# Kernel optimization log

Measured on AMD Instinct MI355X. Metric: run time of the kernel, lower is better.

Reference implementation:

```python
import jax, jax.numpy as jnp
import numpy as np

DIM = 1024
H = 16
HD = DIM // H  # 64
B, N = 2, 2048
EPS = 1e-6


def setup_inputs() -> dict:
    key = jax.random.key(0)
    ks = jax.random.split(key, 12)
    s = 0.02
    return {
        "x": jax.random.normal(ks[0], (B, N, DIM), jnp.float32),
        "rotary_cos": jax.random.uniform(ks[1], (B, N, HD), jnp.float32),
        "rotary_sin": jax.random.uniform(ks[2], (B, N, HD), jnp.float32),
        "Wq": jax.random.normal(ks[3], (DIM, DIM), jnp.float32) * s,
        "bq": jnp.zeros((DIM,), jnp.float32),
        "Wk": jax.random.normal(ks[4], (DIM, DIM), jnp.float32) * s,
        "bk": jnp.zeros((DIM,), jnp.float32),
        "Wv": jax.random.normal(ks[5], (DIM, DIM), jnp.float32) * s,
        "bv": jnp.zeros((DIM,), jnp.float32),
        "q_norm_w": jnp.ones((HD,), jnp.float32),
        "q_norm_b": jnp.zeros((HD,), jnp.float32),
        "k_norm_w": jnp.ones((HD,), jnp.float32),
        "k_norm_b": jnp.zeros((HD,), jnp.float32),
        "Wo": jax.random.normal(ks[6], (DIM, DIM), jnp.float32) * s,
        "bo": jnp.zeros((DIM,), jnp.float32),
    }


def _layernorm(x, w, b):
    mu = jnp.mean(x, axis=-1, keepdims=True)
    var = jnp.mean(jnp.square(x - mu), axis=-1, keepdims=True)
    return (x - mu) * jax.lax.rsqrt(var + EPS) * w + b


def _rotate_half(x):
    x1, x2 = jnp.split(x, 2, axis=-1)
    return jnp.concatenate((-x2, x1), axis=-1)


def _apply_rope(x, cos, sin):
    # x: [B,H,N,D]; cos/sin: [B,N,D] -> [B,1,N,D]
    cos = cos[:, None]
    sin = sin[:, None]
    return x * cos + _rotate_half(x) * sin


def reference(x, rotary_cos, rotary_sin, Wq, bq, Wk, bk, Wv, bv,
              q_norm_w, q_norm_b, k_norm_w, k_norm_b, Wo, bo):
    b, n, c = x.shape
    q = x @ Wq + bq
    k = x @ Wk + bk
    v = x @ Wv + bv
    # Faithful packed-qkv permutation: cat -> view(.., H, 3*hd) -> split(hd)
    qkv = jnp.concatenate((q, k, v), axis=-1).reshape(b, n, H, 3 * HD)
    q, k, v = jnp.split(qkv, 3, axis=-1)  # each [B,N,H,HD]
    q = q.transpose(0, 2, 1, 3)  # [B,H,N,HD]
    k = k.transpose(0, 2, 1, 3)
    v = v.transpose(0, 2, 1, 3)
    q = _layernorm(q, q_norm_w, q_norm_b)
    k = _layernorm(k, k_norm_w, k_norm_b)
    q = _apply_rope(q, rotary_cos, rotary_sin)
    k = _apply_rope(k, rotary_cos, rotary_sin)
    scale = HD ** -0.5
    scores = jnp.einsum("bhqd,bhkd->bhqk", q, k) * scale
    probs = jax.nn.softmax(scores, axis=-1)
    out = jnp.einsum("bhqk,bhkd->bhqd", probs, v)
    out = out.transpose(0, 2, 1, 3).reshape(b, n, c)
    return out @ Wo + bo
```

## Files before the change

### kernel.cpp

```cpp
#include <hip/hip_runtime.h>

typedef __attribute__((ext_vector_type(8))) __bf16 bf16x8;
typedef __attribute__((ext_vector_type(4))) float  f32x4;

#define DEV __device__ __forceinline__

DEV void async_copy16(const void* g, void* l) {
  __builtin_amdgcn_global_load_lds((const __attribute__((address_space(1))) void*)g,
                                   (__attribute__((address_space(3))) void*)l, 16, 0, 0);
}

DEV float ldf(const void* p, size_t i, int isbf) {
  if (isbf) {
    unsigned int w = ((unsigned int)((const unsigned short*)p)[i]) << 16;
    float f; __builtin_memcpy(&f, &w, 4); return f;
  }
  return ((const float*)p)[i];
}

DEV int detect_isbf(const unsigned short* __restrict__ x) {
  int bad = 0;
#pragma unroll
  for (int i = 0; i < 64; i++) {
    int e = (x[i] >> 7) & 0xFF;
    bad |= (e >= 0x90) ? 1 : 0;
  }
  return !bad;
}

__global__ __launch_bounds__(256) void prep(const void* __restrict__ Wq,
                                            const void* __restrict__ Wk,
                                            const void* __restrict__ Wv,
                                            const void* __restrict__ Wo,
                                            const void* __restrict__ x,
                                            const void* __restrict__ bq,
                                            const void* __restrict__ bk,
                                            const void* __restrict__ bv,
                                            const void* __restrict__ bo,
                                            __bf16* __restrict__ Wt,
                                            __bf16* __restrict__ Wot,
                                            __bf16* __restrict__ x_bf,
                                            float* __restrict__ bias) {
  __shared__ float tile[32][33];
  const int isbf = detect_isbf((const unsigned short*)x);
  const int tid = threadIdx.x;
  const int z = blockIdx.z;

  if (z < 4) {
    const void* in = (z == 0) ? Wq : (z == 1) ? Wk : (z == 2) ? Wv : Wo;
    __bf16* out = (z < 3) ? (Wt + (size_t)z * 1024 * 1024) : Wot;
    const int tx = tid & 31, ty = tid >> 5;
    const int r0 = blockIdx.y * 32, c0 = blockIdx.x * 32;
#pragma unroll
    for (int i = 0; i < 4; i++) {
      int r = ty + i * 8;
      tile[r][tx] = ldf(in, (size_t)(r0 + r) * 1024 + c0 + tx, isbf);
    }
    __syncthreads();
#pragma unroll
    for (int i = 0; i < 4; i++) {
      int r = ty + i * 8;
      out[(size_t)(c0 + r) * 1024 + r0 + tx] = (__bf16)tile[tx][r];
    }
  } else {
    const int id = blockIdx.y * 32 + blockIdx.x;
    if (!isbf) {
#pragma unroll
      for (int j = 0; j < 4; j++) {
        int idx = id * 1024 + j * 256 + tid;
        float4 f = ((const float4*)x)[idx];
        union { __bf16 h[4]; uint2 u; } pk;
        pk.h[0] = (__bf16)f.x; pk.h[1] = (__bf16)f.y;
        pk.h[2] = (__bf16)f.z; pk.h[3] = (__bf16)f.w;
        ((uint2*)x_bf)[idx] = pk.u;
      }
    }
    if (id < 16) {
      int i = id * 256 + tid;
      if (i < 1024)      bias[i] = ldf(bq, i, isbf);
      else if (i < 2048) bias[i] = ldf(bk, i - 1024, isbf);
      else if (i < 3072) bias[i] = ldf(bv, i - 2048, isbf);
      else               bias[i] = ldf(bo, i - 3072, isbf);
    }
  }
}

template <int DYN, int NT, int ALT>
__global__ __launch_bounds__(256, 3) void gemm_bt(const __bf16* __restrict__ A,
                                                  const __bf16* __restrict__ Aalt,
                                                  const __bf16* __restrict__ Bt,
                                                  const float* __restrict__ bias,
                                                  void* __restrict__ Cout,
                                                  const unsigned short* __restrict__ xdet,
                                                  int M, int N, int K) {
  constexpr int WN = NT / 2;
  constexpr int JB = WN / 16;
  constexpr int NR = NT / 32;
  __shared__ __align__(16) __bf16 As[128 * 64];
  __shared__ __align__(16) __bf16 Bs[NT * 64];
  const int tid = threadIdx.x;
  const int wid = tid >> 6, lane = tid & 63;
  const int m_blk = blockIdx.x * 128, n_blk = blockIdx.y * NT;
  const int wm = (wid & 1) * 64, wn = (wid >> 1) * WN;
  const int l8 = lane >> 3, l7 = lane & 7;
  const int cc = l7 ^ (l8 & 7);
  const int q4 = lane >> 4, l15 = lane & 15;

  int isbf = 1;
  if (DYN || ALT) isbf = detect_isbf(xdet);
  const __bf16* Ap = (ALT && isbf) ? Aalt : A;

  f32x4 acc[4][JB] = {};

  for (int kb = 0; kb < K; kb += 64) {
    __syncthreads();
#pragma unroll
    for (int i = 0; i < 4; i++) {
      int row = i * 32 + wid * 8 + l8;
      async_copy16(Ap + (size_t)(m_blk + row) * K + kb + cc * 8,
                   As + (i * 32 + wid * 8) * 64);
    }
#pragma unroll
    for (int i = 0; i < NR; i++) {
      int row = i * 32 + wid * 8 + l8;
      async_copy16(Bt + (size_t)(n_blk + row) * K + kb + cc * 8,
                   Bs + (i * 32 + wid * 8) * 64);
    }
    __syncthreads();
#pragma unroll
    for (int k0 = 0; k0 < 64; k0 += 32) {
      bf16x8 a[4], b[JB];
#pragma unroll
      for (int i = 0; i < 4; i++) {
        int ra = wm + i * 16 + l15;
        int ba = ra * 8 + (((k0 >> 3) + q4) ^ (ra & 7));
        a[i] = *(const bf16x8*)&As[ba * 8];
      }
#pragma unroll
      for (int j = 0; j < JB; j++) {
        int rb = wn + j * 16 + l15;
        int bb = rb * 8 + (((k0 >> 3) + q4) ^ (rb & 7));
        b[j] = *(const bf16x8*)&Bs[bb * 8];
      }
#pragma unroll
      for (int i = 0; i < 4; i++)
#pragma unroll
        for (int j = 0; j < JB; j++)
          acc[i][j] = __builtin_amdgcn_mfma_f32_16x16x32_bf16(a[i], b[j], acc[i][j], 0, 0, 0);
    }
  }

  float bcol[JB];
#pragma unroll
  for (int j = 0; j < JB; j++) bcol[j] = bias[n_blk + wn + j * 16 + l15];
#pragma unroll
  for (int i = 0; i < 4; i++)
#pragma unroll
    for (int j = 0; j < JB; j++) {
      int col = n_blk + wn + j * 16 + l15;
#pragma unroll
      for (int r = 0; r < 4; r++) {
        int row = m_blk + wm + i * 16 + q4 * 4 + r;
        float v = acc[i][j][r] + bcol[j];
        size_t idx = (size_t)row * N + col;
        if (DYN && !isbf) ((float*)Cout)[idx] = v;
        else              ((__bf16*)Cout)[idx] = (__bf16)v;
      }
    }
}

__global__ __launch_bounds__(256) void ln_rope_v(const __bf16* __restrict__ qkv,
                                                 const void* __restrict__ rcos,
                                                 const void* __restrict__ rsin,
                                                 const void* __restrict__ qw,
                                                 const void* __restrict__ qb,
                                                 const void* __restrict__ kw,
                                                 const void* __restrict__ kb_,
                                                 const unsigned short* __restrict__ xdet,
                                                 __bf16* __restrict__ Qp,
                                                 __bf16* __restrict__ Kp,
                                                 __bf16* __restrict__ Vt) {
  __shared__ __bf16 vt[64][68];
  const int isbf = detect_isbf(xdet);
  const int tid = threadIdx.x, w = tid >> 6, lane = tid & 63;
  const int bh = blockIdx.y, h = bh & 15, b = bh >> 4;
  const int n0 = blockIdx.x * 64;

  float gq = ldf(qw, lane, isbf), bq_ = ldf(qb, lane, isbf);
  float gk = ldf(kw, lane, isbf), bk_ = ldf(kb_, lane, isbf);

#pragma unroll 2
  for (int t = 0; t < 16; t++) {
    const int n = n0 + w * 16 + t;
    const size_t tok = (size_t)b * 2048 + n;
    const __bf16* base = qkv + tok * 3072 + h * 192;
    float qv = (float)base[lane], kv = (float)base[64 + lane], vv = (float)base[128 + lane];

    float sq = qv, sk = kv;
#pragma unroll
    for (int m = 1; m < 64; m <<= 1) { sq += __shfl_xor(sq, m, 64); sk += __shfl_xor(sk, m, 64); }
    float muq = sq * (1.0f / 64.0f), muk = sk * (1.0f / 64.0f);
    float tq = qv - muq, tk = kv - muk;
    float vq = tq * tq, vk = tk * tk;
#pragma unroll
    for (int m = 1; m < 64; m <<= 1) { vq += __shfl_xor(vq, m, 64); vk += __shfl_xor(vk, m, 64); }
    float rsq = rsqrtf(vq * (1.0f / 64.0f) + 1e-6f);
    float rsk = rsqrtf(vk * (1.0f / 64.0f) + 1e-6f);
    float qn = tq * rsq * gq + bq_;
    float kn = tk * rsk * gk + bk_;

    float c = ldf(rcos, tok * 64 + lane, isbf), s = ldf(rsin, tok * 64 + lane, isbf);
    float qpart = __shfl_xor(qn, 32, 64), kpart = __shfl_xor(kn, 32, 64);
    float qrh = (lane < 32) ? -qpart : qpart;
    float krh = (lane < 32) ? -kpart : kpart;

    const size_t oidx = ((size_t)bh * 2048 + n) * 64 + lane;
    Qp[oidx] = (__bf16)((qn * c + qrh * s) * 0.1803368801111204f);
    Kp[oidx] = (__bf16)(kn * c + krh * s);
    vt[lane][w * 16 + t] = (__bf16)vv;
  }
  __syncthreads();
  const int row = tid >> 2, qt = tid & 3;
  size_t gbase = (size_t)bh * 64 * 2048 + (size_t)row * 2048 + n0 + qt * 16;
#pragma unroll
  for (int u = 0; u < 4; u++)
    *(uint2*)&Vt[gbase + u * 4] = *(const uint2*)&vt[row][qt * 16 + u * 4];
}

__global__ __launch_bounds__(256, 4) void attn(const __bf16* __restrict__ Qp,
                                               const __bf16* __restrict__ Kp,
                                               const __bf16* __restrict__ Vt,
                                               float* __restrict__ O0,
                                               float* __restrict__ O1,
                                               float* __restrict__ lpart) {
  __shared__ __align__(16) __bf16 sK[2][2048];
  __shared__ __align__(16) __bf16 sV[2][2048];
  __shared__ __align__(16) __bf16 sP[4][1024];

  const int tid = threadIdx.x, wid = tid >> 6, lane = tid & 63;
  const int q4 = lane >> 4, l15 = lane & 15;
  const int lin = blockIdx.x;
  const int xcd = lin & 7;
  const int rest = lin >> 3;
  const int qblk = rest & 15;
  const int g = (rest >> 4) * 8 + xcd;
  const int bh = g & 31, split = g >> 5;
  const int q0w = qblk * 128 + wid * 32;
  const int kt0 = split * 1024;
  const __bf16* Qb = Qp + (size_t)bh * 2048 * 64;
  const __bf16* Kb = Kp + (size_t)bh * 2048 * 64;
  const __bf16* Vb = Vt + (size_t)bh * 64 * 2048;
  float* Op = split ? O1 : O0;
  __bf16* sPw = &sP[wid][0];
  const int pbase = (q4 >> 1) * 128 + l15 * 8 + (q4 & 1) * 4;

  bf16x8 qf[2][2];
#pragma unroll
  for (int qs = 0; qs < 2; qs++)
#pragma unroll
    for (int c = 0; c < 2; c++)
      qf[qs][c] = *(const bf16x8*)&Qb[(size_t)(q0w + qs * 16 + l15) * 64 + c * 32 + q4 * 8];

  bf16x8 ones8;
#pragma unroll
  for (int i = 0; i < 8; i++) ones8[i] = (__bf16)1.0f;

  f32x4 o[2][4] = {};
  f32x4 l_acc[2] = {};

#define STAGE(kt, bf)                                                                    \
  do {                                                                                   \
    async_copy16(Kb + (size_t)((kt) + (wid >> 1) * 16 + l15) * 64 + (wid & 1) * 32 + q4 * 8, \
                 &sK[bf][wid * 512]);                                                    \
    async_copy16(Vb + (size_t)(wid * 16 + l15) * 2048 + (kt) + q4 * 8,                   \
                 &sV[bf][wid * 512]);                                                    \
  } while (0)

  STAGE(kt0, 0);

  for (int it = 0; it < 32; ++it) {
    const int buf = it & 1;
    __syncthreads();
    if (it < 31) STAGE(kt0 + (it + 1) * 32, buf ^ 1);

    bf16x8 ak[2][2];
#pragma unroll
    for (int ks = 0; ks < 2; ks++)
#pragma unroll
      for (int c = 0; c < 2; c++)
        ak[ks][c] = *(const bf16x8*)&sK[buf][((ks * 2 + c) * 64 + lane) * 8];
    f32x4 sc[2][2];
#pragma unroll
    for (int qs = 0; qs < 2; qs++)
#pragma unroll
      for (int ks = 0; ks < 2; ks++) {
        f32x4 z = {0.f, 0.f, 0.f, 0.f};
        z = __builtin_amdgcn_mfma_f32_16x16x32_bf16(ak[ks][0], qf[qs][0], z, 0, 0, 0);
        z = __builtin_amdgcn_mfma_f32_16x16x32_bf16(ak[ks][1], qf[qs][1], z, 0, 0, 0);
        sc[qs][ks] = z;
      }

#pragma unroll
    for (int qs = 0; qs < 2; qs++)
#pragma unroll
      for (int ks = 0; ks < 2; ks++) {
        uint2 pk;
        {
          float p0 = __builtin_amdgcn_exp2f(sc[qs][ks][0]);
          float p1 = __builtin_amdgcn_exp2f(sc[qs][ks][1]);
          pk.x = __builtin_amdgcn_perm(__builtin_bit_cast(unsigned int, p1),
                                       __builtin_bit_cast(unsigned int, p0), 0x07060302u);
          float p2 = __builtin_amdgcn_exp2f(sc[qs][ks][2]);
          float p3 = __builtin_amdgcn_exp2f(sc[qs][ks][3]);
          pk.y = __builtin_amdgcn_perm(__builtin_bit_cast(unsigned int, p3),
                                       __builtin_bit_cast(unsigned int, p2), 0x07060302u);
        }
        *(uint2*)&sPw[qs * 512 + ks * 256 + pbase] = pk;
      }
    asm volatile("s_waitcnt lgkmcnt(0)" ::: "memory");

    bf16x8 pb[2];
#pragma unroll
    for (int qs = 0; qs < 2; qs++)
      pb[qs] = *(const bf16x8*)&sPw[(qs * 64 + lane) * 8];
#pragma unroll
    for (int qs = 0; qs < 2; qs++)
      l_acc[qs] = __builtin_amdgcn_mfma_f32_16x16x32_bf16(ones8, pb[qs], l_acc[qs], 0, 0, 0);
#pragma unroll
    for (int ds = 0; ds < 4; ds++) {
      bf16x8 av = *(const bf16x8*)&sV[buf][(ds * 64 + lane) * 8];
#pragma unroll
      for (int qs = 0; qs < 2; qs++)
        o[qs][ds] = __builtin_amdgcn_mfma_f32_16x16x32_bf16(av, pb[qs], o[qs][ds], 0, 0, 0);
    }
  }
#undef STAGE

#pragma unroll
  for (int qs = 0; qs < 2; qs++) {
    const int q = q0w + qs * 16 + l15;
    if (q4 == 0) lpart[(size_t)(split * 32 + bh) * 2048 + q] = l_acc[qs][0];
    size_t base = ((size_t)bh * 2048 + q) * 64;
#pragma unroll
    for (int ds = 0; ds < 4; ds++)
      *(f32x4*)&Op[base + ds * 16 + q4 * 4] = o[qs][ds];
  }
}

__global__ __launch_bounds__(256) void combine(const float* __restrict__ O0,
                                               const float* __restrict__ O1,
                                               const float* __restrict__ lpart,
                                               __bf16* __restrict__ Obuf) {
  const int idx = blockIdx.x * 256 + threadIdx.x;
  const int d4 = idx & 15, q = (idx >> 4) & 2047, bh = idx >> 15;
  const int b = bh >> 4, h = bh & 15;
  const size_t po = ((size_t)bh * 2048 + q) * 64 + d4 * 4;
  f32x4 a = *(const f32x4*)&O0[po];
  f32x4 c = *(const f32x4*)&O1[po];
  float l = lpart[(size_t)bh * 2048 + q] + lpart[(size_t)(32 + bh) * 2048 + q];
  float rl = 1.0f / l;
  union { __bf16 h4[4]; uint2 u; } pk;
#pragma unroll
  for (int r = 0; r < 4; r++) pk.h4[r] = (__bf16)((a[r] + c[r]) * rl);
  *(uint2*)&Obuf[((size_t)(b * 2048 + q)) * 1024 + h * 64 + d4 * 4] = pk.u;
}

extern "C" void kernel_launch(void* const* d_in, const int* in_sizes, int n_in,
                              void* d_out, int out_size, void* d_ws, size_t ws_size,
                              hipStream_t stream) {
  const void* x   = d_in[0];
  const void* rc  = d_in[1];
  const void* rs  = d_in[2];
  const void* Wq  = d_in[3];
  const void* bq  = d_in[4];
  const void* Wk  = d_in[5];
  const void* bk  = d_in[6];
  const void* Wv  = d_in[7];
  const void* bv  = d_in[8];
  const void* qnw = d_in[9];
  const void* qnb = d_in[10];
  const void* knw = d_in[11];
  const void* knb = d_in[12];
  const void* Wo  = d_in[13];
  const void* bo  = d_in[14];
  const unsigned short* xdet = (const unsigned short*)x;

  char* ws = (char*)d_ws;
  __bf16* qkv   = (__bf16*)ws;
  float*  O0    = (float*)ws;
  float*  O1    = (float*)(ws + 16777216);
  __bf16* x_bf  = (__bf16*)(ws + 25165824);
  __bf16* Qp    = (__bf16*)(ws + 33554432);
  __bf16* Obuf  = (__bf16*)(ws + 33554432);
  __bf16* Kp    = (__bf16*)(ws + 41943040);
  __bf16* Vt    = (__bf16*)(ws + 50331648);
  __bf16* Wt    = (__bf16*)(ws + 58720256);
  __bf16* Wot   = (__bf16*)(ws + 65011712);
  float*  bias  = (float*)(ws + 67108864);
  float*  lprt  = (float*)(ws + 67125248);

  prep<<<dim3(32, 32, 5), 256, 0, stream>>>(Wq, Wk, Wv, Wo, x, bq, bk, bv, bo,
                                            Wt, Wot, x_bf, bias);
  gemm_bt<0, 128, 1><<<dim3(32, 24), 256, 0, stream>>>(x_bf, (const __bf16*)x, Wt, bias,
                                                       qkv, xdet, 4096, 3072, 1024);
  ln_rope_v<<<dim3(32, 32), 256, 0, stream>>>(qkv, rc, rs, qnw, qnb, knw, knb, xdet,
                                              Qp, Kp, Vt);
  attn<<<1024, 256, 0, stream>>>(Qp, Kp, Vt, O0, O1, lprt);
  combine<<<4096, 256, 0, stream>>>(O0, O1, lprt, Obuf);
  gemm_bt<1, 64, 0><<<dim3(32, 16), 256, 0, stream>>>(Obuf, nullptr, Wot, bias + 3072,
                                                      d_out, xdet, 4096, 1024, 1024);
}
```

Before: 235.4 us.

## Double attention query tile per wave and remap GEMM blocks by XCD

The attention kernel now gives each wave 64 query rows instead of 32, which halves the grid and reuses each staged K/V tile across twice as many queries. It also fuses the score MFMA with the exp/pack step per sub-tile. Both GEMMs switch to a 1D grid whose block index is remapped so each XCD works on a contiguous range of N columns, which should improve L2 reuse of weight tiles. The costs are more accumulator registers and a larger P buffer in attention, so occupancy drops (launch bound 2 instead of 4), and there are fewer blocks to hide latency.

```diff
diff --git a/kernel.cpp b/kernel.cpp
--- a/kernel.cpp
+++ b/kernel.cpp
@@ -85,7 +85,7 @@
   }
 }
 
-template <int DYN, int NT, int ALT>
+template <int DYN, int NT, int ALT, int NPX>
 __global__ __launch_bounds__(256, 3) void gemm_bt(const __bf16* __restrict__ A,
                                                   const __bf16* __restrict__ Aalt,
                                                   const __bf16* __restrict__ Bt,
@@ -100,7 +100,9 @@
   __shared__ __align__(16) __bf16 Bs[NT * 64];
   const int tid = threadIdx.x;
   const int wid = tid >> 6, lane = tid & 63;
-  const int m_blk = blockIdx.x * 128, n_blk = blockIdx.y * NT;
+  const int xcd = blockIdx.x & 7, t = blockIdx.x >> 3;
+  const int m_blk = (t & 31) * 128;
+  const int n_blk = (xcd * NPX + (t >> 5)) * NT;
   const int wm = (wid & 1) * 64, wn = (wid >> 1) * WN;
   const int l8 = lane >> 3, l7 = lane & 7;
   const int cc = l7 ^ (l8 & 7);
@@ -227,7 +229,7 @@
     *(uint2*)&Vt[gbase + u * 4] = *(const uint2*)&vt[row][qt * 16 + u * 4];
 }
 
-__global__ __launch_bounds__(256, 4) void attn(const __bf16* __restrict__ Qp,
+__global__ __launch_bounds__(256, 2) void attn(const __bf16* __restrict__ Qp,
                                                const __bf16* __restrict__ Kp,
                                                const __bf16* __restrict__ Vt,
                                                float* __restrict__ O0,
@@ -235,17 +237,15 @@
                                                float* __restrict__ lpart) {
   __shared__ __align__(16) __bf16 sK[2][2048];
   __shared__ __align__(16) __bf16 sV[2][2048];
-  __shared__ __align__(16) __bf16 sP[4][1024];
+  __shared__ __align__(16) __bf16 sP[4][2048];
 
   const int tid = threadIdx.x, wid = tid >> 6, lane = tid & 63;
   const int q4 = lane >> 4, l15 = lane & 15;
-  const int lin = blockIdx.x;
-  const int xcd = lin & 7;
-  const int rest = lin >> 3;
-  const int qblk = rest & 15;
-  const int g = (rest >> 4) * 8 + xcd;
+  const int xcd = blockIdx.x & 7, t = blockIdx.x >> 3;
+  const int qblk = t & 7;
+  const int g = xcd * 8 + (t >> 3);
   const int bh = g & 31, split = g >> 5;
-  const int q0w = qblk * 128 + wid * 32;
+  const int q0w = qblk * 256 + wid * 64;
   const int kt0 = split * 1024;
   const __bf16* Qb = Qp + (size_t)bh * 2048 * 64;
   const __bf16* Kb = Kp + (size_t)bh * 2048 * 64;
@@ -254,9 +254,9 @@
   __bf16* sPw = &sP[wid][0];
   const int pbase = (q4 >> 1) * 128 + l15 * 8 + (q4 & 1) * 4;
 
-  bf16x8 qf[2][2];
-#pragma unroll
-  for (int qs = 0; qs < 2; qs++)
+  bf16x8 qf[4][2];
+#pragma unroll
+  for (int qs = 0; qs < 4; qs++)
 #pragma unroll
     for (int c = 0; c < 2; c++)
       qf[qs][c] = *(const bf16x8*)&Qb[(size_t)(q0w + qs * 16 + l15) * 64 + c * 32 + q4 * 8];
@@ -265,8 +265,8 @@
 #pragma unroll
   for (int i = 0; i < 8; i++) ones8[i] = (__bf16)1.0f;
 
-  f32x4 o[2][4] = {};
-  f32x4 l_acc[2] = {};
+  f32x4 o[4][4] = {};
+  f32x4 l_acc[4] = {};
 
 #define STAGE(kt, bf)                                                                    \
   do {                                                                                   \
@@ -289,55 +289,49 @@
 #pragma unroll
       for (int c = 0; c < 2; c++)
         ak[ks][c] = *(const bf16x8*)&sK[buf][((ks * 2 + c) * 64 + lane) * 8];
-    f32x4 sc[2][2];
-#pragma unroll
-    for (int qs = 0; qs < 2; qs++)
+
+#pragma unroll
+    for (int qs = 0; qs < 4; qs++) {
 #pragma unroll
       for (int ks = 0; ks < 2; ks++) {
         f32x4 z = {0.f, 0.f, 0.f, 0.f};
         z = __builtin_amdgcn_mfma_f32_16x16x32_bf16(ak[ks][0], qf[qs][0], z, 0, 0, 0);
         z = __builtin_amdgcn_mfma_f32_16x16x32_bf16(ak[ks][1], qf[qs][1], z, 0, 0, 0);
-        sc[qs][ks] = z;
-      }
-
-#pragma unroll
-    for (int qs = 0; qs < 2; qs++)
-#pragma unroll
-      for (int ks = 0; ks < 2; ks++) {
         uint2 pk;
         {
-          float p0 = __builtin_amdgcn_exp2f(sc[qs][ks][0]);
-          float p1 = __builtin_amdgcn_exp2f(sc[qs][ks][1]);
+          float p0 = __builtin_amdgcn_exp2f(z[0]);
+          float p1 = __builtin_amdgcn_exp2f(z[1]);
           pk.x = __builtin_amdgcn_perm(__builtin_bit_cast(unsigned int, p1),
                                        __builtin_bit_cast(unsigned int, p0), 0x07060302u);
-          float p2 = __builtin_amdgcn_exp2f(sc[qs][ks][2]);
-          float p3 = __builtin_amdgcn_exp2f(sc[qs][ks][3]);
+          float p2 = __builtin_amdgcn_exp2f(z[2]);
+          float p3 = __builtin_amdgcn_exp2f(z[3]);
           pk.y = __builtin_amdgcn_perm(__builtin_bit_cast(unsigned int, p3),
                                        __builtin_bit_cast(unsigned int, p2), 0x07060302u);
         }
         *(uint2*)&sPw[qs * 512 + ks * 256 + pbase] = pk;
       }
+    }
     asm volatile("s_waitcnt lgkmcnt(0)" ::: "memory");
 
-    bf16x8 pb[2];
-#pragma unroll
-    for (int qs = 0; qs < 2; qs++)
+    bf16x8 pb[4];
+#pragma unroll
+    for (int qs = 0; qs < 4; qs++)
       pb[qs] = *(const bf16x8*)&sPw[(qs * 64 + lane) * 8];
 #pragma unroll
-    for (int qs = 0; qs < 2; qs++)
+    for (int qs = 0; qs < 4; qs++)
       l_acc[qs] = __builtin_amdgcn_mfma_f32_16x16x32_bf16(ones8, pb[qs], l_acc[qs], 0, 0, 0);
 #pragma unroll
     for (int ds = 0; ds < 4; ds++) {
       bf16x8 av = *(const bf16x8*)&sV[buf][(ds * 64 + lane) * 8];
 #pragma unroll
-      for (int qs = 0; qs < 2; qs++)
+      for (int qs = 0; qs < 4; qs++)
         o[qs][ds] = __builtin_amdgcn_mfma_f32_16x16x32_bf16(av, pb[qs], o[qs][ds], 0, 0, 0);
     }
   }
 #undef STAGE
 
 #pragma unroll
-  for (int qs = 0; qs < 2; qs++) {
+  for (int qs = 0; qs < 4; qs++) {
     const int q = q0w + qs * 16 + l15;
     if (q4 == 0) lpart[(size_t)(split * 32 + bh) * 2048 + q] = l_acc[qs][0];
     size_t base = ((size_t)bh * 2048 + q) * 64;
@@ -401,12 +395,12 @@
 
   prep<<<dim3(32, 32, 5), 256, 0, stream>>>(Wq, Wk, Wv, Wo, x, bq, bk, bv, bo,
                                             Wt, Wot, x_bf, bias);
-  gemm_bt<0, 128, 1><<<dim3(32, 24), 256, 0, stream>>>(x_bf, (const __bf16*)x, Wt, bias,
-                                                       qkv, xdet, 4096, 3072, 1024);
+  gemm_bt<0, 128, 1, 3><<<768, 256, 0, stream>>>(x_bf, (const __bf16*)x, Wt, bias,
+                                                 qkv, xdet, 4096, 3072, 1024);
   ln_rope_v<<<dim3(32, 32), 256, 0, stream>>>(qkv, rc, rs, qnw, qnb, knw, knb, xdet,
                                               Qp, Kp, Vt);
-  attn<<<1024, 256, 0, stream>>>(Qp, Kp, Vt, O0, O1, lprt);
+  attn<<<512, 256, 0, stream>>>(Qp, Kp, Vt, O0, O1, lprt);
   combine<<<4096, 256, 0, stream>>>(O0, O1, lprt, Obuf);
-  gemm_bt<1, 64, 0><<<dim3(32, 16), 256, 0, stream>>>(Obuf, nullptr, Wot, bias + 3072,
-                                                      d_out, xdet, 4096, 1024, 1024);
-}
+  gemm_bt<1, 64, 0, 2><<<512, 256, 0, stream>>>(Obuf, nullptr, Wot, bias + 3072,
+                                                d_out, xdet, 4096, 1024, 1024);
+}
```

Result: no change. 239.1 us (+1.6%).

## Fuse LayerNorm, RoPE and V transpose into QKV GEMM epilogue with per-head tiles

Applied to the files above, without the earlier changes.

The QKV projection GEMM now uses 128x192 tiles that each cover exactly one head's q, k and v columns. Per-head LayerNorm, RoPE, scaling and the V transpose run in the epilogue from registers, which removes the separate ln_rope_v kernel and the round-trip of the bf16 qkv intermediate through memory. Both GEMMs also switch to a 1-D grid swizzled by XCD so blocks that share weight columns land on the same XCD for L2 reuse. In exchange the QKV kernel holds a larger accumulator (2x12 tiles) and runs at lower occupancy (launch bounds 2), and only 512 blocks are launched.

```diff
diff --git a/kernel.cpp b/kernel.cpp
--- a/kernel.cpp
+++ b/kernel.cpp
@@ -85,9 +85,158 @@
   }
 }
 
-template <int DYN, int NT, int ALT>
+__global__ __launch_bounds__(256, 2) void gemm_qkv(const __bf16* __restrict__ A,
+                                                   const __bf16* __restrict__ Aalt,
+                                                   const __bf16* __restrict__ Bt,
+                                                   const float* __restrict__ bias,
+                                                   const void* __restrict__ rcos,
+                                                   const void* __restrict__ rsin,
+                                                   const void* __restrict__ qnw,
+                                                   const void* __restrict__ qnb,
+                                                   const void* __restrict__ knw,
+                                                   const void* __restrict__ knb,
+                                                   const unsigned short* __restrict__ xdet,
+                                                   __bf16* __restrict__ Qp,
+                                                   __bf16* __restrict__ Kp,
+                                                   __bf16* __restrict__ Vt) {
+  __shared__ __align__(16) __bf16 As[128 * 64];
+  __shared__ __align__(16) __bf16 Bs[192 * 64];
+  const int tid = threadIdx.x, wid = tid >> 6, lane = tid & 63;
+  const int l8 = lane >> 3, l7 = lane & 7;
+  const int cc = l7 ^ (l8 & 7);
+  const int q4 = lane >> 4, l15 = lane & 15;
+
+  const int xcd = blockIdx.x & 7, t = blockIdx.x >> 3;
+  const int m_blk = (t & 31) * 128;
+  const int h = xcd * 2 + (t >> 5);
+  const int n_blk = h * 192;
+
+  const int isbf = detect_isbf(xdet);
+  const __bf16* Ap = isbf ? Aalt : A;
+  const int K = 1024;
+
+  f32x4 acc[2][12] = {};
+
+  for (int kb = 0; kb < K; kb += 64) {
+    __syncthreads();
+#pragma unroll
+    for (int i = 0; i < 4; i++) {
+      int row = i * 32 + wid * 8 + l8;
+      async_copy16(Ap + (size_t)(m_blk + row) * K + kb + cc * 8,
+                   As + (i * 32 + wid * 8) * 64);
+    }
+#pragma unroll
+    for (int i = 0; i < 6; i++) {
+      int row = i * 32 + wid * 8 + l8;
+      async_copy16(Bt + (size_t)(n_blk + row) * K + kb + cc * 8,
+                   Bs + (i * 32 + wid * 8) * 64);
+    }
+    __syncthreads();
+#pragma unroll
+    for (int k0 = 0; k0 < 64; k0 += 32) {
+      bf16x8 a[2], b[12];
+#pragma unroll
+      for (int i = 0; i < 2; i++) {
+        int ra = wid * 32 + i * 16 + l15;
+        int ba = ra * 8 + (((k0 >> 3) + q4) ^ (ra & 7));
+        a[i] = *(const bf16x8*)&As[ba * 8];
+      }
+#pragma unroll
+      for (int j = 0; j < 12; j++) {
+        int rb = j * 16 + l15;
+        int bb = rb * 8 + (((k0 >> 3) + q4) ^ (rb & 7));
+        b[j] = *(const bf16x8*)&Bs[bb * 8];
+      }
+#pragma unroll
+      for (int i = 0; i < 2; i++)
+#pragma unroll
+        for (int j = 0; j < 12; j++)
+          acc[i][j] = __builtin_amdgcn_mfma_f32_16x16x32_bf16(a[i], b[j], acc[i][j], 0, 0, 0);
+    }
+  }
+
+  float bc[12], gq[4], bq4[4], gk[4], bk4[4];
+#pragma unroll
+  for (int j = 0; j < 12; j++) bc[j] = bias[n_blk + j * 16 + l15];
+#pragma unroll
+  for (int j = 0; j < 4; j++) {
+    gq[j]  = ldf(qnw, j * 16 + l15, isbf);
+    bq4[j] = ldf(qnb, j * 16 + l15, isbf);
+    gk[j]  = ldf(knw, j * 16 + l15, isbf);
+    bk4[j] = ldf(knb, j * 16 + l15, isbf);
+  }
+
+  __syncthreads();
+  __bf16* vt = (__bf16*)Bs;
+
+#pragma unroll
+  for (int i = 0; i < 2; i++) {
+#pragma unroll
+    for (int r = 0; r < 4; r++) {
+      const int rowl = wid * 32 + i * 16 + q4 * 4 + r;
+      const int m = m_blk + rowl;
+      const int b = m >> 11, n = m & 2047;
+      const size_t tok = (size_t)b * 2048 + n;
+
+      float qv[4], kv[4];
+#pragma unroll
+      for (int j = 0; j < 4; j++) { qv[j] = acc[i][j][r] + bc[j]; kv[j] = acc[i][4 + j][r] + bc[4 + j]; }
+      float sq = qv[0] + qv[1] + qv[2] + qv[3];
+      float sk = kv[0] + kv[1] + kv[2] + kv[3];
+#pragma unroll
+      for (int mk = 1; mk < 16; mk <<= 1) { sq += __shfl_xor(sq, mk, 64); sk += __shfl_xor(sk, mk, 64); }
+      float muq = sq * (1.0f / 64.0f), muk = sk * (1.0f / 64.0f);
+      float vq = 0.f, vk = 0.f;
+#pragma unroll
+      for (int j = 0; j < 4; j++) {
+        float u = qv[j] - muq; qv[j] = u; vq += u * u;
+        float w = kv[j] - muk; kv[j] = w; vk += w * w;
+      }
+#pragma unroll
+      for (int mk = 1; mk < 16; mk <<= 1) { vq += __shfl_xor(vq, mk, 64); vk += __shfl_xor(vk, mk, 64); }
+      float rsq = rsqrtf(vq * (1.0f / 64.0f) + 1e-6f);
+      float rsk = rsqrtf(vk * (1.0f / 64.0f) + 1e-6f);
+
+      float qn[4], kn[4], cs[4], sn[4];
+#pragma unroll
+      for (int j = 0; j < 4; j++) {
+        qn[j] = qv[j] * rsq * gq[j] + bq4[j];
+        kn[j] = kv[j] * rsk * gk[j] + bk4[j];
+        cs[j] = ldf(rcos, tok * 64 + j * 16 + l15, isbf);
+        sn[j] = ldf(rsin, tok * 64 + j * 16 + l15, isbf);
+      }
+      const size_t ob = ((size_t)(b * 16 + h) * 2048 + n) * 64;
+#pragma unroll
+      for (int j = 0; j < 2; j++) {
+        float qr0 = qn[j] * cs[j] - qn[j + 2] * sn[j];
+        float qr1 = qn[j + 2] * cs[j + 2] + qn[j] * sn[j + 2];
+        float kr0 = kn[j] * cs[j] - kn[j + 2] * sn[j];
+        float kr1 = kn[j + 2] * cs[j + 2] + kn[j] * sn[j + 2];
+        Qp[ob + j * 16 + l15]       = (__bf16)(qr0 * 0.1803368801111204f);
+        Qp[ob + (j + 2) * 16 + l15] = (__bf16)(qr1 * 0.1803368801111204f);
+        Kp[ob + j * 16 + l15]       = (__bf16)kr0;
+        Kp[ob + (j + 2) * 16 + l15] = (__bf16)kr1;
+      }
+#pragma unroll
+      for (int j = 0; j < 4; j++) {
+        int d = j * 16 + l15;
+        vt[d * 132 + rowl] = (__bf16)(acc[i][8 + j][r] + bc[8 + j]);
+      }
+    }
+  }
+  __syncthreads();
+  {
+    const int d = tid >> 2, qt = tid & 3;
+    const int b0 = m_blk >> 11, n0 = m_blk & 2047;
+    size_t gbase = ((size_t)(b0 * 16 + h) * 64 + d) * 2048 + n0 + qt * 32;
+#pragma unroll
+    for (int u = 0; u < 8; u++)
+      *(uint2*)&Vt[gbase + u * 4] = *(const uint2*)&vt[d * 132 + qt * 32 + u * 4];
+  }
+}
+
+template <int DYN, int NT, int NPX>
 __global__ __launch_bounds__(256, 3) void gemm_bt(const __bf16* __restrict__ A,
-                                                  const __bf16* __restrict__ Aalt,
                                                   const __bf16* __restrict__ Bt,
                                                   const float* __restrict__ bias,
                                                   void* __restrict__ Cout,
@@ -100,15 +249,16 @@
   __shared__ __align__(16) __bf16 Bs[NT * 64];
   const int tid = threadIdx.x;
   const int wid = tid >> 6, lane = tid & 63;
-  const int m_blk = blockIdx.x * 128, n_blk = blockIdx.y * NT;
+  const int xcd = blockIdx.x & 7, t = blockIdx.x >> 3;
+  const int m_blk = (t & 31) * 128;
+  const int n_blk = (xcd * NPX + (t >> 5)) * NT;
   const int wm = (wid & 1) * 64, wn = (wid >> 1) * WN;
   const int l8 = lane >> 3, l7 = lane & 7;
   const int cc = l7 ^ (l8 & 7);
   const int q4 = lane >> 4, l15 = lane & 15;
 
   int isbf = 1;
-  if (DYN || ALT) isbf = detect_isbf(xdet);
-  const __bf16* Ap = (ALT && isbf) ? Aalt : A;
+  if (DYN) isbf = detect_isbf(xdet);
 
   f32x4 acc[4][JB] = {};
 
@@ -117,7 +267,7 @@
 #pragma unroll
     for (int i = 0; i < 4; i++) {
       int row = i * 32 + wid * 8 + l8;
-      async_copy16(Ap + (size_t)(m_blk + row) * K + kb + cc * 8,
+      async_copy16(A + (size_t)(m_blk + row) * K + kb + cc * 8,
                    As + (i * 32 + wid * 8) * 64);
     }
 #pragma unroll
@@ -167,64 +317,6 @@
         else              ((__bf16*)Cout)[idx] = (__bf16)v;
       }
     }
-}
-
-__global__ __launch_bounds__(256) void ln_rope_v(const __bf16* __restrict__ qkv,
-                                                 const void* __restrict__ rcos,
-                                                 const void* __restrict__ rsin,
-                                                 const void* __restrict__ qw,
-                                                 const void* __restrict__ qb,
-                                                 const void* __restrict__ kw,
-                                                 const void* __restrict__ kb_,
-                                                 const unsigned short* __restrict__ xdet,
-                                                 __bf16* __restrict__ Qp,
-                                                 __bf16* __restrict__ Kp,
-                                                 __bf16* __restrict__ Vt) {
-  __shared__ __bf16 vt[64][68];
-  const int isbf = detect_isbf(xdet);
-  const int tid = threadIdx.x, w = tid >> 6, lane = tid & 63;
-  const int bh = blockIdx.y, h = bh & 15, b = bh >> 4;
-  const int n0 = blockIdx.x * 64;
-
-  float gq = ldf(qw, lane, isbf), bq_ = ldf(qb, lane, isbf);
-  float gk = ldf(kw, lane, isbf), bk_ = ldf(kb_, lane, isbf);
-
-#pragma unroll 2
-  for (int t = 0; t < 16; t++) {
-    const int n = n0 + w * 16 + t;
-    const size_t tok = (size_t)b * 2048 + n;
-    const __bf16* base = qkv + tok * 3072 + h * 192;
-    float qv = (float)base[lane], kv = (float)base[64 + lane], vv = (float)base[128 + lane];
-
-    float sq = qv, sk = kv;
-#pragma unroll
-    for (int m = 1; m < 64; m <<= 1) { sq += __shfl_xor(sq, m, 64); sk += __shfl_xor(sk, m, 64); }
-    float muq = sq * (1.0f / 64.0f), muk = sk * (1.0f / 64.0f);
-    float tq = qv - muq, tk = kv - muk;
-    float vq = tq * tq, vk = tk * tk;
-#pragma unroll
-    for (int m = 1; m < 64; m <<= 1) { vq += __shfl_xor(vq, m, 64); vk += __shfl_xor(vk, m, 64); }
-    float rsq = rsqrtf(vq * (1.0f / 64.0f) + 1e-6f);
-    float rsk = rsqrtf(vk * (1.0f / 64.0f) + 1e-6f);
-    float qn = tq * rsq * gq + bq_;
-    float kn = tk * rsk * gk + bk_;
-
-    float c = ldf(rcos, tok * 64 + lane, isbf), s = ldf(rsin, tok * 64 + lane, isbf);
-    float qpart = __shfl_xor(qn, 32, 64), kpart = __shfl_xor(kn, 32, 64);
-    float qrh = (lane < 32) ? -qpart : qpart;
-    float krh = (lane < 32) ? -kpart : kpart;
-
-    const size_t oidx = ((size_t)bh * 2048 + n) * 64 + lane;
-    Qp[oidx] = (__bf16)((qn * c + qrh * s) * 0.1803368801111204f);
-    Kp[oidx] = (__bf16)(kn * c + krh * s);
-    vt[lane][w * 16 + t] = (__bf16)vv;
-  }
-  __syncthreads();
-  const int row = tid >> 2, qt = tid & 3;
-  size_t gbase = (size_t)bh * 64 * 2048 + (size_t)row * 2048 + n0 + qt * 16;
-#pragma unroll
-  for (int u = 0; u < 4; u++)
-    *(uint2*)&Vt[gbase + u * 4] = *(const uint2*)&vt[row][qt * 16 + u * 4];
 }
 
 __global__ __launch_bounds__(256, 4) void attn(const __bf16* __restrict__ Qp,
@@ -386,7 +478,6 @@
   const unsigned short* xdet = (const unsigned short*)x;
 
   char* ws = (char*)d_ws;
-  __bf16* qkv   = (__bf16*)ws;
   float*  O0    = (float*)ws;
   float*  O1    = (float*)(ws + 16777216);
   __bf16* x_bf  = (__bf16*)(ws + 25165824);
@@ -401,12 +492,10 @@
 
   prep<<<dim3(32, 32, 5), 256, 0, stream>>>(Wq, Wk, Wv, Wo, x, bq, bk, bv, bo,
                                             Wt, Wot, x_bf, bias);
-  gemm_bt<0, 128, 1><<<dim3(32, 24), 256, 0, stream>>>(x_bf, (const __bf16*)x, Wt, bias,
-                                                       qkv, xdet, 4096, 3072, 1024);
-  ln_rope_v<<<dim3(32, 32), 256, 0, stream>>>(qkv, rc, rs, qnw, qnb, knw, knb, xdet,
-                                              Qp, Kp, Vt);
+  gemm_qkv<<<512, 256, 0, stream>>>(x_bf, (const __bf16*)x, Wt, bias, rc, rs,
+                                    qnw, qnb, knw, knb, xdet, Qp, Kp, Vt);
   attn<<<1024, 256, 0, stream>>>(Qp, Kp, Vt, O0, O1, lprt);
   combine<<<4096, 256, 0, stream>>>(O0, O1, lprt, Obuf);
-  gemm_bt<1, 64, 0><<<dim3(32, 16), 256, 0, stream>>>(Obuf, nullptr, Wot, bias + 3072,
-                                                      d_out, xdet, 4096, 1024, 1024);
-}
+  gemm_bt<1, 64, 2><<<512, 256, 0, stream>>>(Obuf, Wot, bias + 3072,
+                                             d_out, xdet, 4096, 1024, 1024);
+}
```

Result: faster. 218.2 us (-7.3%).
